# Kernel optimization log

Hardware: AMD Instinct MI355X
Metric: run time of the kernel (lower is better)

Reference implementation:

```python
import jax, jax.numpy as jnp
import numpy as np

B, S, H = 2, 2048, 1024
NH, HD = 16, 64
SCALE = HD ** -0.5


def setup_inputs() -> dict:
    key = jax.random.key(0)
    k1, k2, k3, k4 = jax.random.split(key, 4)
    hidden_states = jax.random.normal(k1, (B, S, H), dtype=jnp.float32)
    attention_mask = jax.random.randint(k2, (B, S), 0, 2, dtype=jnp.int32)
    # xavier-uniform-ish init scale
    w_qkv = jax.random.normal(k3, (3 * H, H), dtype=jnp.float32) * (2.0 / (H + 3 * H)) ** 0.5
    w_out = jax.random.normal(k4, (H, H), dtype=jnp.float32) * (1.0 / H) ** 0.5
    return {"hidden_states": hidden_states, "attention_mask": attention_mask,
            "w_qkv": w_qkv, "w_out": w_out}


def reference(hidden_states, attention_mask, w_qkv, w_out):
    b, s, _ = hidden_states.shape
    qkv = hidden_states @ w_qkv.T                      # [B,S,3H]
    q, k, v = jnp.split(qkv, 3, axis=-1)
    # [B,S,H] -> [B,NH,S,HD]
    reshape = lambda x: x.reshape(b, s, NH, HD).transpose(0, 2, 1, 3)
    q, k, v = reshape(q), reshape(k), reshape(v)
    scores = jnp.einsum('bhqd,bhkd->bhqk', q, k) * SCALE   # [B,NH,S,S]
    mask = attention_mask[:, None, None, :] == 0           # [B,1,1,S]
    scores = jnp.where(mask, -jnp.inf, scores)
    attn = jax.nn.softmax(scores, axis=-1)                 # dropout p: eval mode -> identity
    out = jnp.einsum('bhqk,bhkd->bhqd', attn, v)           # [B,NH,S,HD]
    out = out.transpose(0, 2, 1, 3).reshape(b, s, H)
    return out @ w_out.T
```

## Files before the change

### kernel.cpp

```cpp
#include <hip/hip_runtime.h>
#include <string.h>


typedef __bf16    bf16x8 __attribute__((ext_vector_type(8)));
typedef _Float16  f16x4  __attribute__((ext_vector_type(4)));
typedef _Float16  f16x2  __attribute__((ext_vector_type(2)));
typedef float     f32x4  __attribute__((ext_vector_type(4)));

#define NTOK   4096
#define HDIM   1024
#define SEQ    2048
#define NHEAD  16
#define F2SHIFT 4.0f
#define QSCALE  0.18033688f
#define LSTRIDE 68

__device__ __forceinline__ float bf2f(unsigned short u) {
    union { unsigned int i; float f; } x;
    x.i = ((unsigned int)u) << 16;
    return x.f;
}
__device__ __forceinline__ unsigned short f2bf(float f) {
    union { __bf16 h; unsigned short u; } x;
    x.h = (__bf16)f;
    return x.u;
}
__device__ __forceinline__ unsigned short f2h(float f) {
    union { _Float16 h; unsigned short u; } x;
    x.h = (_Float16)f;
    return x.u;
}
__device__ __forceinline__ f16x2 pkrtz(float a, float b) {
    union { __fp16 __attribute__((ext_vector_type(2))) i; f16x2 o; } x;
    x.i = __builtin_amdgcn_cvt_pkrtz(a, b);
    return x.o;
}

__device__ __forceinline__ int detect_f32(const unsigned short* hs) {
    unsigned int idx = (threadIdx.x & 63) * 4096u;
    float f = bf2f(hs[idx]);
    return __any(!(fabsf(f) < 1e4f));
}

typedef const __attribute__((address_space(1))) unsigned int* gptr_u32;
typedef __attribute__((address_space(3))) unsigned int* lptr_u32;

__device__ __forceinline__ void async16(const unsigned short* g, unsigned short* l) {
    __builtin_amdgcn_global_load_lds((gptr_u32)g, (lptr_u32)l, 16, 0, 0);
}

__global__ void convert3_kernel(const void* __restrict__ s0, const void* __restrict__ s1,
                                const void* __restrict__ s2, unsigned short* __restrict__ dst) {
    const int isf32 = detect_f32((const unsigned short*)s0);
    if (!isf32) return;
    int g = blockIdx.x * blockDim.x + threadIdx.x;
    const int stride = gridDim.x * blockDim.x;
    for (; g < 1048576; g += stride) {
        int i = g * 8;
        const void* src; int off;
        if (i < 4194304)      { src = s0; off = i; }
        else if (i < 7340032) { src = s1; off = i - 4194304; }
        else                  { src = s2; off = i - 7340032; }
        const float* s = (const float*)src + off;
        unsigned short o[8];
#pragma unroll
        for (int j = 0; j < 8; j++) o[j] = f2bf(s[j]);
        *(uint4*)(dst + i) = *(const uint4*)o;
    }
}

__global__ __launch_bounds__(256) void gemm_qkv(
    const unsigned short* __restrict__ Xc, const unsigned short* __restrict__ Wc,
    const unsigned short* __restrict__ Xraw, const unsigned short* __restrict__ Wraw,
    unsigned short* __restrict__ q_out, unsigned short* __restrict__ k_out,
    unsigned short* __restrict__ v_out) {
    const int K = 1024;
    __shared__ __align__(16) unsigned short Xs[128 * 32];
    __shared__ __align__(16) unsigned short Ws[128 * 32];

    const int isf32 = detect_f32(Xraw);
    const unsigned short* X = isf32 ? Xc : Xraw;
    const unsigned short* W = isf32 ? Wc : Wraw;

    const int t = threadIdx.x;
    const int w = t >> 6, lane = t & 63, quad = lane >> 4, lr = lane & 15;
    const int wrow = (w >> 1) * 64, wcol = (w & 1) * 64;
    const int m0 = blockIdx.y * 128, n0 = blockIdx.x * 128;
    const bool vblk = (n0 >= 2048);

    f32x4 acc[4][4];
#pragma unroll
    for (int mi = 0; mi < 4; mi++)
#pragma unroll
        for (int ni = 0; ni < 4; ni++) acc[mi][ni] = (f32x4){0.f, 0.f, 0.f, 0.f};

    const int srow = w * 32 + (lane >> 2);
    const int scol = (lane & 3) * 8;
    const unsigned short* xg = X + (size_t)(m0 + srow) * K + scol;
    const unsigned short* wg = W + (size_t)(n0 + srow) * K + scol;
    unsigned short* xl0 = &Xs[w * 1024];
    unsigned short* wl0 = &Ws[w * 1024];

    for (int k0 = 0; k0 < K; k0 += 32) {
        __syncthreads();
        async16(xg + k0, xl0);
        async16(xg + k0 + 16 * K, xl0 + 512);
        async16(wg + k0, wl0);
        async16(wg + k0 + 16 * K, wl0 + 512);
        __syncthreads();
        bf16x8 af[4], bfr[4];
#pragma unroll
        for (int mi = 0; mi < 4; mi++)
            af[mi] = *(bf16x8*)&Xs[(wrow + mi * 16 + lr) * 32 + quad * 8];
#pragma unroll
        for (int ni = 0; ni < 4; ni++)
            bfr[ni] = *(bf16x8*)&Ws[(wcol + ni * 16 + lr) * 32 + quad * 8];
        if (!vblk) {
#pragma unroll
            for (int mi = 0; mi < 4; mi++)
#pragma unroll
                for (int ni = 0; ni < 4; ni++)
                    acc[mi][ni] = __builtin_amdgcn_mfma_f32_16x16x32_bf16(af[mi], bfr[ni], acc[mi][ni], 0, 0, 0);
        } else {
#pragma unroll
            for (int mi = 0; mi < 4; mi++)
#pragma unroll
                for (int ni = 0; ni < 4; ni++)
                    acc[mi][ni] = __builtin_amdgcn_mfma_f32_16x16x32_bf16(bfr[ni], af[mi], acc[mi][ni], 0, 0, 0);
        }
    }

    if (!vblk) {
#pragma unroll
        for (int mi = 0; mi < 4; mi++)
#pragma unroll
            for (int ni = 0; ni < 4; ni++)
#pragma unroll
                for (int rr = 0; rr < 4; rr++) {
                    int mrow = m0 + wrow + mi * 16 + quad * 4 + rr;
                    int j = n0 + wcol + ni * 16 + lr;
                    float val = acc[mi][ni][rr];
                    int which = j >> 10, rem = j & 1023;
                    int nh = rem >> 6, hd = rem & 63;
                    int b = mrow >> 11, s = mrow & 2047;
                    size_t dst = ((size_t)(b * NHEAD + nh) * SEQ + s) * 64 + hd;
                    if (which == 0) q_out[dst] = f2bf(val * QSCALE);
                    else            k_out[dst] = f2bf(val);
                }
    } else {
#pragma unroll
        for (int mi = 0; mi < 4; mi++)
#pragma unroll
            for (int ni = 0; ni < 4; ni++)
#pragma unroll
                for (int rr = 0; rr < 4; rr++) {
                    int n = n0 + wcol + ni * 16 + quad * 4 + rr;
                    int m = m0 + wrow + mi * 16 + lr;
                    float val = acc[mi][ni][rr];
                    int rem = n & 1023;
                    int nh = rem >> 6, hd = rem & 63;
                    int b = m >> 11, s = m & 2047;
                    size_t dst = ((size_t)(b * NHEAD + nh) * 64 + hd) * SEQ + s;
                    v_out[dst] = f2h(val);
                }
    }
}

__global__ __launch_bounds__(256) void gemm_out(
    const unsigned short* __restrict__ X, const unsigned short* __restrict__ Wc,
    const unsigned short* __restrict__ Wraw,
    void* __restrict__ d_out, const unsigned short* __restrict__ hs_raw) {
    const int K = 1024, N = 1024;
    __shared__ __align__(16) unsigned short Xs[64 * 32];
    __shared__ __align__(16) unsigned short Ws[128 * 32];

    const int isf32 = detect_f32(hs_raw);
    const unsigned short* W = isf32 ? Wc : Wraw;

    const int t = threadIdx.x;
    const int w = t >> 6, lane = t & 63, quad = lane >> 4, lr = lane & 15;
    const int wrow = (w >> 1) * 32, wcol = (w & 1) * 64;
    const int m0 = blockIdx.y * 64, n0 = blockIdx.x * 128;

    f32x4 acc[2][4];
#pragma unroll
    for (int mi = 0; mi < 2; mi++)
#pragma unroll
        for (int ni = 0; ni < 4; ni++) acc[mi][ni] = (f32x4){0.f, 0.f, 0.f, 0.f};

    const int sxrow = w * 16 + (lane >> 2);
    const int swrow = w * 32 + (lane >> 2);
    const int scol = (lane & 3) * 8;
    const unsigned short* xg = X + (size_t)(m0 + sxrow) * K + scol;
    const unsigned short* wg = W + (size_t)(n0 + swrow) * K + scol;
    unsigned short* xl0 = &Xs[w * 512];
    unsigned short* wl0 = &Ws[w * 1024];

    for (int k0 = 0; k0 < K; k0 += 32) {
        __syncthreads();
        async16(xg + k0, xl0);
        async16(wg + k0, wl0);
        async16(wg + k0 + 16 * K, wl0 + 512);
        __syncthreads();
        bf16x8 af[2], bfr[4];
#pragma unroll
        for (int mi = 0; mi < 2; mi++)
            af[mi] = *(bf16x8*)&Xs[(wrow + mi * 16 + lr) * 32 + quad * 8];
#pragma unroll
        for (int ni = 0; ni < 4; ni++)
            bfr[ni] = *(bf16x8*)&Ws[(wcol + ni * 16 + lr) * 32 + quad * 8];
#pragma unroll
        for (int mi = 0; mi < 2; mi++)
#pragma unroll
            for (int ni = 0; ni < 4; ni++)
                acc[mi][ni] = __builtin_amdgcn_mfma_f32_16x16x32_bf16(af[mi], bfr[ni], acc[mi][ni], 0, 0, 0);
    }

#pragma unroll
    for (int mi = 0; mi < 2; mi++)
#pragma unroll
        for (int ni = 0; ni < 4; ni++)
#pragma unroll
            for (int rr = 0; rr < 4; rr++) {
                int mrow = m0 + wrow + mi * 16 + quad * 4 + rr;
                int j = n0 + wcol + ni * 16 + lr;
                float val = acc[mi][ni][rr];
                size_t dst = (size_t)mrow * N + j;
                if (isf32) ((float*)d_out)[dst] = val;
                else ((unsigned short*)d_out)[dst] = f2bf(val);
            }
}

__global__ __launch_bounds__(256) void flash_attn_v7(
    const unsigned short* __restrict__ q, const unsigned short* __restrict__ k,
    const unsigned short* __restrict__ vt, const int* __restrict__ mask,
    unsigned short* __restrict__ attn_out) {
    __shared__ __align__(16) unsigned short Ks[64 * LSTRIDE];
    __shared__ __align__(16) unsigned short Vt[64 * LSTRIDE];
    __shared__ __align__(16) float Msk[80];

    const int t = threadIdx.x;
    const int w = t >> 6, lane = t & 63, quad = lane >> 4, lr = lane & 15;
    const int bh = blockIdx.x, b = bh >> 4, h = bh & 15;
    const int q0 = blockIdx.y * 128;

    const unsigned short* qb = q + (size_t)bh * SEQ * 64;
    const unsigned short* kb = k + (size_t)bh * SEQ * 64;
    const unsigned short* vtb = vt + (size_t)bh * 64 * SEQ;
    const int* mb = mask + b * SEQ;

    bf16x8 qf[2][2];
#pragma unroll
    for (int qg = 0; qg < 2; qg++) {
        const unsigned short* qrow = qb + (size_t)(q0 + w * 32 + qg * 16 + lr) * 64 + quad * 8;
        qf[qg][0] = *(const bf16x8*)qrow;
        qf[qg][1] = *(const bf16x8*)(qrow + 32);
    }

    f32x4 oacc[2][4];
#pragma unroll
    for (int qg = 0; qg < 2; qg++)
#pragma unroll
        for (int dt = 0; dt < 4; dt++) oacc[qg][dt] = (f32x4){0.f, 0.f, 0.f, 0.f};
    float l_st[2] = {0.f, 0.f};

    const int sr = t >> 2;
    const int sc = (t & 3) * 16;

    for (int kk0 = 0; kk0 < SEQ; kk0 += 64) {
        const uint4* kp = (const uint4*)(kb + (size_t)(kk0 + sr) * 64 + sc);
        const uint4* vp = (const uint4*)(vtb + (size_t)sr * SEQ + kk0 + sc);
        uint4 ka = kp[0], kb2 = kp[1];
        uint4 va = vp[0], vb2 = vp[1];
        float mval = 0.f;
        if (t < 64) mval = (mb[kk0 + t] == 0) ? -1e30f : -F2SHIFT;

        __syncthreads();
        *(uint4*)&Ks[sr * LSTRIDE + sc] = ka;
        *(uint4*)&Ks[sr * LSTRIDE + sc + 8] = kb2;
        *(uint4*)&Vt[sr * LSTRIDE + sc] = va;
        *(uint4*)&Vt[sr * LSTRIDE + sc + 8] = vb2;
        if (t < 64) Msk[t] = mval;
        __syncthreads();

#pragma unroll
        for (int mt = 0; mt < 4; mt++) {
            bf16x8 a1h0 = *(bf16x8*)&Ks[(mt * 16 + lr) * LSTRIDE + quad * 8];
            bf16x8 a1h1 = *(bf16x8*)&Ks[(mt * 16 + lr) * LSTRIDE + 32 + quad * 8];
            f16x4 a2[4];
#pragma unroll
            for (int dt = 0; dt < 4; dt++)
                a2[dt] = *(f16x4*)&Vt[(dt * 16 + lr) * LSTRIDE + mt * 16 + quad * 4];
            float4 mv = *(const float4*)&Msk[mt * 16 + quad * 4];

#pragma unroll
            for (int qg = 0; qg < 2; qg++) {
                f32x4 z = (f32x4){0.f, 0.f, 0.f, 0.f};
                z = __builtin_amdgcn_mfma_f32_16x16x32_bf16(a1h0, qf[qg][0], z, 0, 0, 0);
                z = __builtin_amdgcn_mfma_f32_16x16x32_bf16(a1h1, qf[qg][1], z, 0, 0, 0);
                float p0 = __builtin_amdgcn_exp2f(z[0] + mv.x);
                float p1 = __builtin_amdgcn_exp2f(z[1] + mv.y);
                float p2 = __builtin_amdgcn_exp2f(z[2] + mv.z);
                float p3 = __builtin_amdgcn_exp2f(z[3] + mv.w);
                l_st[qg] += (p0 + p1) + (p2 + p3);
                f16x2 ab = pkrtz(p0, p1);
                f16x2 cd = pkrtz(p2, p3);
                f16x4 b2;
                b2[0] = ab[0]; b2[1] = ab[1]; b2[2] = cd[0]; b2[3] = cd[1];
#pragma unroll
                for (int dt = 0; dt < 4; dt++)
                    oacc[qg][dt] = __builtin_amdgcn_mfma_f32_16x16x16f16(a2[dt], b2, oacc[qg][dt], 0, 0, 0);
            }
        }
    }

    float inv[2];
#pragma unroll
    for (int qg = 0; qg < 2; qg++) {
        float s = l_st[qg];
        s += __shfl_xor(s, 16);
        s += __shfl_xor(s, 32);
        inv[qg] = 1.0f / s;
    }
#pragma unroll
    for (int qg = 0; qg < 2; qg++) {
        size_t tok = (size_t)(b * SEQ + q0 + w * 32 + qg * 16 + lr);
#pragma unroll
        for (int dt = 0; dt < 4; dt++)
#pragma unroll
            for (int rr = 0; rr < 4; rr++)
                attn_out[tok * HDIM + h * 64 + dt * 16 + quad * 4 + rr] =
                    f2bf(oacc[qg][dt][rr] * inv[qg]);
    }
}

extern "C" void kernel_launch(void* const* d_in, const int* in_sizes, int n_in,
                              void* d_out, int out_size, void* d_ws, size_t ws_size,
                              hipStream_t stream) {
    const void* hs_raw = d_in[0];
    const int* mask = (const int*)d_in[1];
    const void* wqkv_raw = d_in[2];
    const void* wout_raw = d_in[3];

    char* wsb = (char*)d_ws;
    unsigned short* hs_c = (unsigned short*)(wsb + 256);
    unsigned short* wqkv_c = hs_c + 4194304;
    unsigned short* wout_c = wqkv_c + 3145728;
    unsigned short* qw = wout_c + 1048576;
    unsigned short* kw = qw + 4194304;
    unsigned short* vtw = kw + 4194304;
    unsigned short* ao = vtw + 4194304;

    convert3_kernel<<<1024, 256, 0, stream>>>(hs_raw, wqkv_raw, wout_raw, hs_c);

    gemm_qkv<<<dim3(24, 32), 256, 0, stream>>>(hs_c, wqkv_c,
                                               (const unsigned short*)hs_raw,
                                               (const unsigned short*)wqkv_raw,
                                               qw, kw, vtw);
    flash_attn_v7<<<dim3(32, 16), 256, 0, stream>>>(qw, kw, vtw, mask, ao);
    gemm_out<<<dim3(8, 64), 256, 0, stream>>>(ao, wout_c,
                                              (const unsigned short*)wout_raw, d_out,
                                              (const unsigned short*)hs_raw);
}
```

Baseline: 197.1 us.

## Stage QKV GEMM epilogue through LDS for coalesced stores, fold mask into MFMA

The QKV GEMM epilogue now writes the accumulators into a padded shared-memory tile in two passes, then stores 16-byte vectors to Q/K and to transposed V, instead of scattered 2-byte global writes. The attention kernel seeds the score MFMA accumulator with the mask bias, which removes four adds per tile. The convert kernel's grid drops from 1024 to 256 blocks. The epilogue change adds about 17 KB of LDS and extra barriers, which may lower GEMM occupancy.

```diff
diff --git a/kernel.cpp b/kernel.cpp
--- a/kernel.cpp
+++ b/kernel.cpp
@@ -14,6 +14,7 @@
 #define F2SHIFT 4.0f
 #define QSCALE  0.18033688f
 #define LSTRIDE 68
+#define TSTRIDE 66
 
 __device__ __forceinline__ float bf2f(unsigned short u) {
     union { unsigned int i; float f; } x;
@@ -77,6 +78,7 @@
     const int K = 1024;
     __shared__ __align__(16) unsigned short Xs[128 * 32];
     __shared__ __align__(16) unsigned short Ws[128 * 32];
+    __shared__ __align__(16) unsigned short Tr[128 * TSTRIDE];
 
     const int isf32 = detect_f32(Xraw);
     const unsigned short* X = isf32 ? Xc : Xraw;
@@ -131,38 +133,65 @@
     }
 
     if (!vblk) {
-#pragma unroll
-        for (int mi = 0; mi < 4; mi++)
-#pragma unroll
-            for (int ni = 0; ni < 4; ni++)
-#pragma unroll
-                for (int rr = 0; rr < 4; rr++) {
-                    int mrow = m0 + wrow + mi * 16 + quad * 4 + rr;
-                    int j = n0 + wcol + ni * 16 + lr;
-                    float val = acc[mi][ni][rr];
-                    int which = j >> 10, rem = j & 1023;
-                    int nh = rem >> 6, hd = rem & 63;
-                    int b = mrow >> 11, s = mrow & 2047;
-                    size_t dst = ((size_t)(b * NHEAD + nh) * SEQ + s) * 64 + hd;
-                    if (which == 0) q_out[dst] = f2bf(val * QSCALE);
-                    else            k_out[dst] = f2bf(val);
-                }
+        const int isQ = (n0 < 1024);
+        unsigned short* outp = isQ ? q_out : k_out;
+#pragma unroll
+        for (int pass = 0; pass < 2; pass++) {
+            __syncthreads();
+            if ((wcol >> 6) == pass) {
+#pragma unroll
+                for (int mi = 0; mi < 4; mi++)
+#pragma unroll
+                    for (int ni = 0; ni < 4; ni++)
+#pragma unroll
+                        for (int rr = 0; rr < 4; rr++) {
+                            int r = wrow + mi * 16 + quad * 4 + rr;
+                            int c = ni * 16 + lr;
+                            float val = acc[mi][ni][rr];
+                            Tr[r * TSTRIDE + c] = isQ ? f2bf(val * QSCALE) : f2bf(val);
+                        }
+            }
+            __syncthreads();
+            int nh = ((n0 + pass * 64) & 1023) >> 6;
+#pragma unroll
+            for (int it = 0; it < 4; it++) {
+                int r = (t >> 3) + it * 32;
+                int c8 = (t & 7) * 8;
+                uint4 v = *(uint4*)&Tr[r * TSTRIDE + c8];
+                int mrow = m0 + r;
+                int bb = mrow >> 11, s = mrow & 2047;
+                *(uint4*)&outp[((size_t)(bb * NHEAD + nh) * SEQ + s) * 64 + c8] = v;
+            }
+        }
     } else {
 #pragma unroll
-        for (int mi = 0; mi < 4; mi++)
-#pragma unroll
-            for (int ni = 0; ni < 4; ni++)
-#pragma unroll
-                for (int rr = 0; rr < 4; rr++) {
-                    int n = n0 + wcol + ni * 16 + quad * 4 + rr;
-                    int m = m0 + wrow + mi * 16 + lr;
-                    float val = acc[mi][ni][rr];
-                    int rem = n & 1023;
-                    int nh = rem >> 6, hd = rem & 63;
-                    int b = m >> 11, s = m & 2047;
-                    size_t dst = ((size_t)(b * NHEAD + nh) * 64 + hd) * SEQ + s;
-                    v_out[dst] = f2h(val);
-                }
+        for (int pass = 0; pass < 2; pass++) {
+            __syncthreads();
+            if ((wrow >> 6) == pass) {
+#pragma unroll
+                for (int mi = 0; mi < 4; mi++)
+#pragma unroll
+                    for (int ni = 0; ni < 4; ni++)
+#pragma unroll
+                        for (int rr = 0; rr < 4; rr++) {
+                            int cn = wcol + ni * 16 + quad * 4 + rr;
+                            int tk = mi * 16 + lr;
+                            Tr[cn * TSTRIDE + tk] = f2h(acc[mi][ni][rr]);
+                        }
+            }
+            __syncthreads();
+#pragma unroll
+            for (int it = 0; it < 4; it++) {
+                int cn = (t >> 3) + it * 32;
+                int tk8 = (t & 7) * 8;
+                uint4 v = *(uint4*)&Tr[cn * TSTRIDE + tk8];
+                int rem = (n0 + cn) & 1023;
+                int nh = rem >> 6, hd = rem & 63;
+                int m = m0 + pass * 64 + tk8;
+                int bb = m >> 11, s = m & 2047;
+                *(uint4*)&v_out[((size_t)(bb * NHEAD + nh) * 64 + hd) * SEQ + s] = v;
+            }
+        }
     }
 }
 
@@ -231,7 +260,7 @@
             }
 }
 
-__global__ __launch_bounds__(256) void flash_attn_v7(
+__global__ __launch_bounds__(256) void flash_attn_v8(
     const unsigned short* __restrict__ q, const unsigned short* __restrict__ k,
     const unsigned short* __restrict__ vt, const int* __restrict__ mask,
     unsigned short* __restrict__ attn_out) {
@@ -295,13 +324,13 @@
 
 #pragma unroll
             for (int qg = 0; qg < 2; qg++) {
-                f32x4 z = (f32x4){0.f, 0.f, 0.f, 0.f};
+                f32x4 z = (f32x4){mv.x, mv.y, mv.z, mv.w};
                 z = __builtin_amdgcn_mfma_f32_16x16x32_bf16(a1h0, qf[qg][0], z, 0, 0, 0);
                 z = __builtin_amdgcn_mfma_f32_16x16x32_bf16(a1h1, qf[qg][1], z, 0, 0, 0);
-                float p0 = __builtin_amdgcn_exp2f(z[0] + mv.x);
-                float p1 = __builtin_amdgcn_exp2f(z[1] + mv.y);
-                float p2 = __builtin_amdgcn_exp2f(z[2] + mv.z);
-                float p3 = __builtin_amdgcn_exp2f(z[3] + mv.w);
+                float p0 = __builtin_amdgcn_exp2f(z[0]);
+                float p1 = __builtin_amdgcn_exp2f(z[1]);
+                float p2 = __builtin_amdgcn_exp2f(z[2]);
+                float p3 = __builtin_amdgcn_exp2f(z[3]);
                 l_st[qg] += (p0 + p1) + (p2 + p3);
                 f16x2 ab = pkrtz(p0, p1);
                 f16x2 cd = pkrtz(p2, p3);
@@ -351,13 +380,13 @@
     unsigned short* vtw = kw + 4194304;
     unsigned short* ao = vtw + 4194304;
 
-    convert3_kernel<<<1024, 256, 0, stream>>>(hs_raw, wqkv_raw, wout_raw, hs_c);
+    convert3_kernel<<<256, 256, 0, stream>>>(hs_raw, wqkv_raw, wout_raw, hs_c);
 
     gemm_qkv<<<dim3(24, 32), 256, 0, stream>>>(hs_c, wqkv_c,
                                                (const unsigned short*)hs_raw,
                                                (const unsigned short*)wqkv_raw,
                                                qw, kw, vtw);
-    flash_attn_v7<<<dim3(32, 16), 256, 0, stream>>>(qw, kw, vtw, mask, ao);
+    flash_attn_v8<<<dim3(32, 16), 256, 0, stream>>>(qw, kw, vtw, mask, ao);
     gemm_out<<<dim3(8, 64), 256, 0, stream>>>(ao, wout_c,
                                               (const unsigned short*)wout_raw, d_out,
                                               (const unsigned short*)hs_raw);
```

After: 197.8 us. Within noise of the previous version (+0.4%).
